# Kernel optimization log

Hardware: AMD Instinct MI355X
Metric: run time of the kernel (lower is better)

## Reference

```python
import jax, jax.numpy as jnp
import numpy as np

B, L = 4096, 64          # batch, patch_len
OUT, KS, K = 64, 8, 4    # out_planes, kernel_size, num mixtures
STRIDE = 1
TEMP = 34.0
L_OUT = (L - KS) // STRIDE + 1   # 57
C = OUT * L_OUT                  # BN feature dim = 3648
HIDDEN = int(L * 0.5) + 1        # attention hidden planes = 33
EPS = 1e-5


def _gelu(x):
    return jax.nn.gelu(x, approximate=False)  # torch nn.GELU default = exact erf


def setup_inputs() -> dict:
    key = jax.random.key(0)
    ks = jax.random.split(key, 8)
    return {
        "x": jax.random.normal(ks[0], (B, L), jnp.float32),
        "fc1_w": jax.random.normal(ks[1], (HIDDEN, L), jnp.float32) * (2.0 / HIDDEN) ** 0.5,
        "fc2_w": jax.random.normal(ks[2], (K, HIDDEN), jnp.float32) * (2.0 / K) ** 0.5,
        "fc2_b": jnp.zeros((K,), jnp.float32),
        "weight": jax.random.normal(ks[3], (K, OUT, KS), jnp.float32) * 0.1,
        "bias": jnp.zeros((K, OUT), jnp.float32),
        "bn_gamma": jnp.ones((C,), jnp.float32),
        "bn_beta": jnp.zeros((C,), jnp.float32),
    }


def reference(x, fc1_w, fc2_w, fc2_b, weight, bias, bn_gamma, bn_beta):
    # --- attention1d: 1x1 convs over the patch_len 'channel' dim == linears ---
    a = _gelu(x @ fc1_w.T)                 # [B, HIDDEN]
    logits = a @ fc2_w.T + fc2_b           # [B, K]
    attn = jax.nn.softmax(logits / TEMP, axis=1)

    # --- sliding windows (im2col), shared by both conv paths ---
    idx = jnp.arange(L_OUT)[:, None] * STRIDE + jnp.arange(KS)[None, :]
    frames = x[:, idx]                     # [B, L_OUT, KS]

    # --- kernel_wise: full conv with each of the K kernels ---
    kw = jnp.einsum('blc,koc->bolk', frames, weight) + bias.T[None, :, None, :]  # [B,OUT,L_OUT,K]
    kw = kw.reshape(B, C, K)

    # --- per-sample aggregated kernel + grouped (per-sample) conv ---
    agg_w = jnp.einsum('bk,koc->boc', attn, weight)      # [B, OUT, KS]
    agg_b = attn @ bias                                  # [B, OUT]
    out = jnp.einsum('blc,boc->bol', frames, agg_w) + agg_b[:, :, None]  # [B,OUT,L_OUT]
    out = out.reshape(B, C)

    # --- BN(GELU(.)) with batch statistics (training-mode BatchNorm1d) ---
    g = _gelu(out)
    m = g.mean(axis=0)
    v = g.var(axis=0)
    out = (g - m) * jax.lax.rsqrt(v + EPS) * bn_gamma + bn_beta

    g2 = _gelu(kw)                                        # [B, C, K]
    m2 = g2.mean(axis=(0, 2), keepdims=True)
    v2 = g2.var(axis=(0, 2), keepdims=True)
    kw = (g2 - m2) * jax.lax.rsqrt(v2 + EPS) * bn_gamma[None, :, None] + bn_beta[None, :, None]

    return out, attn, kw.transpose(0, 2, 1)              # [B,C], [B,K], [B,K,C]
```

## Files before the change

kernel.cpp:

```cpp
#include <hip/hip_runtime.h>
#include <cstddef>

#define B_     4096
#define L_     64
#define OUT_   64
#define KS_    8
#define KK_    4
#define LOUT_  57
#define C_     3648
#define HID_   33
#define TEMP_  34.0f
#define EPS_   1e-5f
#define NCH_   128
#define SROWS_ 32
#define NB2_   32

__device__ __forceinline__ float gelu_f(float x) {
    float e = exp2f(-2.3022083f * x * fmaf(0.044715f * x, x, 1.0f));
    return x * __builtin_amdgcn_rcpf(1.0f + e);
}

__global__ __launch_bounds__(128) void attn_kernel(
    const float* __restrict__ x, const float* __restrict__ fc1_w,
    const float* __restrict__ fc2_w, const float* __restrict__ fc2_b,
    float* __restrict__ attn_out)
{
    __shared__ float fc1s[HID_][L_];
    __shared__ float fc2s[KK_][HID_];
    __shared__ float fc2bs[KK_];
    int tid = threadIdx.x;
    for (int i = tid; i < HID_ * L_; i += 128) fc1s[i / L_][i % L_] = fc1_w[i];
    for (int i = tid; i < KK_ * HID_; i += 128) fc2s[i / HID_][i % HID_] = fc2_w[i];
    if (tid < KK_) fc2bs[tid] = fc2_b[tid];
    __syncthreads();

    int b = blockIdx.x * 128 + tid;
    if (b >= B_) return;

    float xr[L_];
    const float4* xp = (const float4*)(x + (size_t)b * L_);
    #pragma unroll
    for (int i = 0; i < L_ / 4; ++i) {
        float4 v = xp[i];
        xr[4*i] = v.x; xr[4*i+1] = v.y; xr[4*i+2] = v.z; xr[4*i+3] = v.w;
    }
    float logit[KK_] = {0.f, 0.f, 0.f, 0.f};
    for (int h = 0; h < HID_; ++h) {
        const float4* fr = (const float4*)&fc1s[h][0];
        float acc = 0.f;
        #pragma unroll
        for (int i = 0; i < L_ / 4; ++i) {
            float4 wv = fr[i];
            acc = fmaf(xr[4*i],   wv.x, acc);
            acc = fmaf(xr[4*i+1], wv.y, acc);
            acc = fmaf(xr[4*i+2], wv.z, acc);
            acc = fmaf(xr[4*i+3], wv.w, acc);
        }
        float a = gelu_f(acc);
        #pragma unroll
        for (int k = 0; k < KK_; ++k) logit[k] = fmaf(a, fc2s[k][h], logit[k]);
    }
    float z[KK_];
    #pragma unroll
    for (int k = 0; k < KK_; ++k) z[k] = (logit[k] + fc2bs[k]) * (1.0f / TEMP_);
    float mx = fmaxf(fmaxf(z[0], z[1]), fmaxf(z[2], z[3]));
    float e[KK_]; float s = 0.f;
    #pragma unroll
    for (int k = 0; k < KK_; ++k) { e[k] = __expf(z[k] - mx); s += e[k]; }
    float inv = __builtin_amdgcn_rcpf(s);
    #pragma unroll
    for (int k = 0; k < KK_; ++k) attn_out[(size_t)b * KK_ + k] = e[k] * inv;
}

__global__ __launch_bounds__(256) void stats_kernel(
    const float* __restrict__ x, const float* __restrict__ weight,
    const float* __restrict__ bias, const float* __restrict__ attn,
    float* __restrict__ P, int use_partial)
{
    const int RPC = B_ / NCH_;
    int cb = blockIdx.x;
    int chunk = blockIdx.y;
    int tid = threadIdx.x;
    int c = cb * 256 + tid;
    bool act = c < C_;
    int o = act ? (c / LOUT_) : 0;
    int l = act ? (c - o * LOUT_) : 0;

    float w[KK_][KS_];
    float bk[KK_];
    #pragma unroll
    for (int k = 0; k < KK_; ++k) {
        bk[k] = bias[k * OUT_ + o];
        #pragma unroll
        for (int cq = 0; cq < KS_; ++cq) w[k][cq] = weight[(k * OUT_ + o) * KS_ + cq];
    }

    __shared__ float xs[SROWS_][L_];
    __shared__ float at[SROWS_][KK_];

    float s1 = 0.f, s2 = 0.f, t1 = 0.f, t2 = 0.f;

    for (int round = 0; round < RPC / SROWS_; ++round) {
        int b0 = chunk * RPC + round * SROWS_;
        __syncthreads();
        {
            const float4* xp4 = (const float4*)(x + (size_t)b0 * L_);
            float4* xd = (float4*)&xs[0][0];
            xd[tid] = xp4[tid];
            xd[tid + 256] = xp4[tid + 256];
            if (tid < SROWS_ * KK_) ((float*)at)[tid] = attn[(size_t)b0 * KK_ + tid];
        }
        __syncthreads();
        if (act) {
            #pragma unroll 4
            for (int r = 0; r < SROWS_; ++r) {
                float kv0 = bk[0], kv1 = bk[1], kv2 = bk[2], kv3 = bk[3];
                #pragma unroll
                for (int cq = 0; cq < KS_; ++cq) {
                    float xv = xs[r][l + cq];
                    kv0 = fmaf(xv, w[0][cq], kv0);
                    kv1 = fmaf(xv, w[1][cq], kv1);
                    kv2 = fmaf(xv, w[2][cq], kv2);
                    kv3 = fmaf(xv, w[3][cq], kv3);
                }
                float ov = at[r][0] * kv0;
                ov = fmaf(at[r][1], kv1, ov);
                ov = fmaf(at[r][2], kv2, ov);
                ov = fmaf(at[r][3], kv3, ov);
                float g = gelu_f(ov);
                s1 += g; s2 = fmaf(g, g, s2);
                float g0 = gelu_f(kv0), g1 = gelu_f(kv1), g2 = gelu_f(kv2), g3 = gelu_f(kv3);
                t1 += g0 + g1 + g2 + g3;
                t2 = fmaf(g0, g0, t2); t2 = fmaf(g1, g1, t2);
                t2 = fmaf(g2, g2, t2); t2 = fmaf(g3, g3, t2);
            }
        }
    }
    if (!act) return;
    if (use_partial) {
        size_t base = (size_t)chunk * 4 * C_ + c;
        P[base]          = s1;
        P[base + C_]     = s2;
        P[base + 2 * C_] = t1;
        P[base + 3 * C_] = t2;
    } else {
        atomicAdd(&P[c], s1);
        atomicAdd(&P[C_ + c], s2);
        atomicAdd(&P[2 * C_ + c], t1);
        atomicAdd(&P[3 * C_ + c], t2);
    }
}

__global__ __launch_bounds__(256) void finalize_kernel(
    const float* __restrict__ P, const float* __restrict__ gamma,
    const float* __restrict__ beta, float* __restrict__ F, int use_partial)
{
    __shared__ float red[4][64];
    int t = threadIdx.x;
    int cl = t & 63;
    int s = t >> 6;
    int c = blockIdx.x * 64 + cl;
    float a = 0.f;
    if (use_partial) {
        for (int ch = 0; ch < NCH_; ++ch)
            a += P[((size_t)ch * 4 + s) * C_ + c];
    } else {
        a = P[(size_t)s * C_ + c];
    }
    red[s][cl] = a;
    __syncthreads();
    if (t < 64) {
        float a0 = red[0][cl], a1 = red[1][cl], a2 = red[2][cl], a3 = red[3][cl];
        float m  = a0 * (1.0f / B_);
        float v  = a1 * (1.0f / B_) - m * m;
        float rs = rsqrtf(v + EPS_);
        float m2 = a2 * (1.0f / (B_ * KK_));
        float v2 = a3 * (1.0f / (B_ * KK_)) - m2 * m2;
        float rs2 = rsqrtf(v2 + EPS_);
        float ga = gamma[c], be = beta[c];
        F[c]          = rs * ga;
        F[C_ + c]     = be - m * rs * ga;
        F[2 * C_ + c] = rs2 * ga;
        F[3 * C_ + c] = be - m2 * rs2 * ga;
    }
}

__global__ __launch_bounds__(256) void write_kernel(
    const float* __restrict__ x, const float* __restrict__ weight,
    const float* __restrict__ bias, const float* __restrict__ attn,
    const float* __restrict__ F,
    float* __restrict__ out0, float* __restrict__ kwout)
{
    int cc = blockIdx.x;
    int bg = blockIdx.y;
    int tid = threadIdx.x;
    int c = cc * 256 + tid;
    bool act = c < C_;
    int o = act ? (c / LOUT_) : 0;
    int l = act ? (c - o * LOUT_) : 0;

    float w[KK_][KS_];
    float bk[KK_];
    #pragma unroll
    for (int k = 0; k < KK_; ++k) {
        bk[k] = bias[k * OUT_ + o];
        #pragma unroll
        for (int cq = 0; cq < KS_; ++cq) w[k][cq] = weight[(k * OUT_ + o) * KS_ + cq];
    }
    float sA = 0.f, hA = 0.f, sK = 0.f, hK = 0.f;
    if (act) {
        sA = F[c]; hA = F[C_ + c]; sK = F[2 * C_ + c]; hK = F[3 * C_ + c];
    }

    __shared__ float xs[NB2_][L_];
    __shared__ float at[NB2_][KK_];
    int b0 = bg * NB2_;
    {
        const float4* xp4 = (const float4*)(x + (size_t)b0 * L_);
        float4* xd = (float4*)&xs[0][0];
        xd[tid] = xp4[tid];
        xd[tid + 256] = xp4[tid + 256];
        if (tid < NB2_ * KK_) ((float*)at)[tid] = attn[(size_t)b0 * KK_ + tid];
    }
    __syncthreads();

    if (!act) return;

    #pragma unroll 4
    for (int r = 0; r < NB2_; ++r) {
        float kv0 = bk[0], kv1 = bk[1], kv2 = bk[2], kv3 = bk[3];
        #pragma unroll
        for (int cq = 0; cq < KS_; ++cq) {
            float xv = xs[r][l + cq];
            kv0 = fmaf(xv, w[0][cq], kv0);
            kv1 = fmaf(xv, w[1][cq], kv1);
            kv2 = fmaf(xv, w[2][cq], kv2);
            kv3 = fmaf(xv, w[3][cq], kv3);
        }
        float ov = at[r][0] * kv0;
        ov = fmaf(at[r][1], kv1, ov);
        ov = fmaf(at[r][2], kv2, ov);
        ov = fmaf(at[r][3], kv3, ov);
        int b = b0 + r;
        float g = gelu_f(ov);
        out0[(size_t)b * C_ + c] = fmaf(g, sA, hA);
        float g0 = gelu_f(kv0), g1 = gelu_f(kv1), g2v = gelu_f(kv2), g3 = gelu_f(kv3);
        float* base = kwout + (size_t)b * KK_ * C_ + c;
        base[0]      = fmaf(g0,  sK, hK);
        base[C_]     = fmaf(g1,  sK, hK);
        base[2 * C_] = fmaf(g2v, sK, hK);
        base[3 * C_] = fmaf(g3,  sK, hK);
    }
}

extern "C" void kernel_launch(void* const* d_in, const int* in_sizes, int n_in,
                              void* d_out, int out_size, void* d_ws, size_t ws_size,
                              hipStream_t stream) {
    const float* x      = (const float*)d_in[0];
    const float* fc1_w  = (const float*)d_in[1];
    const float* fc2_w  = (const float*)d_in[2];
    const float* fc2_b  = (const float*)d_in[3];
    const float* weight = (const float*)d_in[4];
    const float* bias   = (const float*)d_in[5];
    const float* gamma  = (const float*)d_in[6];
    const float* beta   = (const float*)d_in[7];

    float* out  = (float*)d_out;
    float* out0 = out;
    float* attn = out + (size_t)B_ * C_;
    float* kwout = attn + (size_t)B_ * KK_;

    size_t need = (size_t)(NCH_ * 4 + 4) * C_ * sizeof(float);
    int use_partial = ws_size >= need;
    float* P = (float*)d_ws;
    float* F = P + (use_partial ? (size_t)NCH_ * 4 * C_ : (size_t)4 * C_);
    if (!use_partial)
        hipMemsetAsync(P, 0, 4 * C_ * sizeof(float), stream);

    attn_kernel<<<B_ / 128, 128, 0, stream>>>(x, fc1_w, fc2_w, fc2_b, attn);
    stats_kernel<<<dim3((C_ + 255) / 256, NCH_), 256, 0, stream>>>(
        x, weight, bias, attn, P, use_partial);
    finalize_kernel<<<C_ / 64, 256, 0, stream>>>(P, gamma, beta, F, use_partial);
    write_kernel<<<dim3((C_ + 255) / 256, B_ / NB2_), 256, 0, stream>>>(
        x, weight, bias, attn, F, out0, kwout);
}
```

Before: 147.2 us.

## Compute four adjacent output positions per thread with vectorized loads and stores

Each thread in the stats and write kernels now handles a tile of four consecutive output positions (15 tiles per output channel, the last holding a single position). It reads three float4 window segments from shared memory and reuses them across the four positions, then writes 16-byte vector stores through an unaligned packed type. The stats kernel drops its inner round loop, so each block covers only 16 rows and there are 256 chunks. The write kernel now uses 16-row groups. The trade-off is higher register pressure and partially idle last tiles, in exchange for fewer shared-memory loads and wider global stores.

```diff
diff --git a/kernel.cpp b/kernel.cpp
--- a/kernel.cpp
+++ b/kernel.cpp
@@ -11,13 +11,35 @@
 #define HID_   33
 #define TEMP_  34.0f
 #define EPS_   1e-5f
-#define NCH_   128
-#define SROWS_ 32
-#define NB2_   32
+#define NCH_   256
+#define SROWS_ 16
+#define NBW_   16
+#define NTILE_ 960
+
+typedef float f32x4 __attribute__((ext_vector_type(4)));
+
+struct __attribute__((packed, aligned(4))) f4u { f32x4 v; };
+__device__ __forceinline__ void store4(float* p, f32x4 v) {
+    reinterpret_cast<f4u*>(p)->v = v;
+}
+__device__ __forceinline__ f32x4 load4(const float* p) {
+    return reinterpret_cast<const f4u*>(p)->v;
+}
 
 __device__ __forceinline__ float gelu_f(float x) {
     float e = exp2f(-2.3022083f * x * fmaf(0.044715f * x, x, 1.0f));
     return x * __builtin_amdgcn_rcpf(1.0f + e);
+}
+
+template<int ROWS>
+__device__ __forceinline__ void stage_rows(
+    const float* __restrict__ x, int b0, int tid, float4 (*xs)[17])
+{
+    for (int idx = tid; idx < ROWS * 17; idx += 256) {
+        int r = idx / 17, t = idx - r * 17;
+        const float4* xrow = (const float4*)(x + (size_t)(b0 + r) * L_);
+        xs[r][t] = xrow[t < 16 ? t : 15];
+    }
 }
 
 __global__ __launch_bounds__(128) void attn_kernel(
@@ -35,7 +57,6 @@
     __syncthreads();
 
     int b = blockIdx.x * 128 + tid;
-    if (b >= B_) return;
 
     float xr[L_];
     const float4* xp = (const float4*)(x + (size_t)b * L_);
@@ -77,14 +98,15 @@
     const float* __restrict__ bias, const float* __restrict__ attn,
     float* __restrict__ P, int use_partial)
 {
-    const int RPC = B_ / NCH_;
-    int cb = blockIdx.x;
+    int tid = threadIdx.x;
+    int tile = blockIdx.x * 256 + tid;
     int chunk = blockIdx.y;
-    int tid = threadIdx.x;
-    int c = cb * 256 + tid;
-    bool act = c < C_;
-    int o = act ? (c / LOUT_) : 0;
-    int l = act ? (c - o * LOUT_) : 0;
+    bool act = tile < NTILE_;
+    int o  = act ? tile / 15 : 0;
+    int lt = act ? tile - o * 15 : 0;
+    int l0 = lt * 4;
+    int c0 = o * LOUT_ + l0;
+    bool full = (lt != 14);
 
     float w[KK_][KS_];
     float bk[KK_];
@@ -92,62 +114,75 @@
     for (int k = 0; k < KK_; ++k) {
         bk[k] = bias[k * OUT_ + o];
         #pragma unroll
-        for (int cq = 0; cq < KS_; ++cq) w[k][cq] = weight[(k * OUT_ + o) * KS_ + cq];
-    }
-
-    __shared__ float xs[SROWS_][L_];
-    __shared__ float at[SROWS_][KK_];
-
-    float s1 = 0.f, s2 = 0.f, t1 = 0.f, t2 = 0.f;
-
-    for (int round = 0; round < RPC / SROWS_; ++round) {
-        int b0 = chunk * RPC + round * SROWS_;
-        __syncthreads();
-        {
-            const float4* xp4 = (const float4*)(x + (size_t)b0 * L_);
-            float4* xd = (float4*)&xs[0][0];
-            xd[tid] = xp4[tid];
-            xd[tid + 256] = xp4[tid + 256];
-            if (tid < SROWS_ * KK_) ((float*)at)[tid] = attn[(size_t)b0 * KK_ + tid];
-        }
-        __syncthreads();
-        if (act) {
-            #pragma unroll 4
-            for (int r = 0; r < SROWS_; ++r) {
-                float kv0 = bk[0], kv1 = bk[1], kv2 = bk[2], kv3 = bk[3];
+        for (int t = 0; t < KS_; ++t) w[k][t] = weight[(k * OUT_ + o) * KS_ + t];
+    }
+
+    __shared__ float4 xs[SROWS_][17];
+    __shared__ float4 at4[SROWS_];
+    int b0 = chunk * SROWS_;
+    stage_rows<SROWS_>(x, b0, tid, xs);
+    if (tid < SROWS_) at4[tid] = *(const float4*)(attn + (size_t)(b0 + tid) * KK_);
+    __syncthreads();
+
+    f32x4 s1 = {0,0,0,0}, s2 = {0,0,0,0}, t1 = {0,0,0,0}, t2 = {0,0,0,0};
+    if (act) {
+        #pragma unroll 2
+        for (int r = 0; r < SROWS_; ++r) {
+            float4 X0 = xs[r][lt], X1 = xs[r][lt+1], X2 = xs[r][lt+2];
+            float xw[12] = {X0.x,X0.y,X0.z,X0.w, X1.x,X1.y,X1.z,X1.w,
+                            X2.x,X2.y,X2.z,X2.w};
+            float4 atv = at4[r];
+            float kv[4][KK_];
+            #pragma unroll
+            for (int e = 0; e < 4; ++e)
                 #pragma unroll
-                for (int cq = 0; cq < KS_; ++cq) {
-                    float xv = xs[r][l + cq];
-                    kv0 = fmaf(xv, w[0][cq], kv0);
-                    kv1 = fmaf(xv, w[1][cq], kv1);
-                    kv2 = fmaf(xv, w[2][cq], kv2);
-                    kv3 = fmaf(xv, w[3][cq], kv3);
+                for (int k = 0; k < KK_; ++k) {
+                    float a = bk[k];
+                    #pragma unroll
+                    for (int t = 0; t < KS_; ++t) a = fmaf(xw[e + t], w[k][t], a);
+                    kv[e][k] = a;
                 }
-                float ov = at[r][0] * kv0;
-                ov = fmaf(at[r][1], kv1, ov);
-                ov = fmaf(at[r][2], kv2, ov);
-                ov = fmaf(at[r][3], kv3, ov);
-                float g = gelu_f(ov);
-                s1 += g; s2 = fmaf(g, g, s2);
-                float g0 = gelu_f(kv0), g1 = gelu_f(kv1), g2 = gelu_f(kv2), g3 = gelu_f(kv3);
-                t1 += g0 + g1 + g2 + g3;
-                t2 = fmaf(g0, g0, t2); t2 = fmaf(g1, g1, t2);
-                t2 = fmaf(g2, g2, t2); t2 = fmaf(g3, g3, t2);
+            f32x4 g4;
+            #pragma unroll
+            for (int e = 0; e < 4; ++e) {
+                float ov = atv.x * kv[e][0];
+                ov = fmaf(atv.y, kv[e][1], ov);
+                ov = fmaf(atv.z, kv[e][2], ov);
+                ov = fmaf(atv.w, kv[e][3], ov);
+                g4[e] = gelu_f(ov);
+            }
+            s1 = s1 + g4;
+            s2 = __builtin_elementwise_fma(g4, g4, s2);
+            #pragma unroll
+            for (int k = 0; k < KK_; ++k) {
+                f32x4 gk;
+                #pragma unroll
+                for (int e = 0; e < 4; ++e) gk[e] = gelu_f(kv[e][k]);
+                t1 = t1 + gk;
+                t2 = __builtin_elementwise_fma(gk, gk, t2);
             }
         }
     }
     if (!act) return;
     if (use_partial) {
-        size_t base = (size_t)chunk * 4 * C_ + c;
-        P[base]          = s1;
-        P[base + C_]     = s2;
-        P[base + 2 * C_] = t1;
-        P[base + 3 * C_] = t2;
+        size_t base = (size_t)chunk * 4 * C_ + c0;
+        if (full) {
+            store4(&P[base], s1);
+            store4(&P[base + C_], s2);
+            store4(&P[base + 2 * C_], t1);
+            store4(&P[base + 3 * C_], t2);
+        } else {
+            P[base] = s1.x; P[base + C_] = s2.x;
+            P[base + 2 * C_] = t1.x; P[base + 3 * C_] = t2.x;
+        }
     } else {
-        atomicAdd(&P[c], s1);
-        atomicAdd(&P[C_ + c], s2);
-        atomicAdd(&P[2 * C_ + c], t1);
-        atomicAdd(&P[3 * C_ + c], t2);
+        int ne = full ? 4 : 1;
+        for (int e = 0; e < ne; ++e) {
+            atomicAdd(&P[c0 + e], s1[e]);
+            atomicAdd(&P[C_ + c0 + e], s2[e]);
+            atomicAdd(&P[2 * C_ + c0 + e], t1[e]);
+            atomicAdd(&P[3 * C_ + c0 + e], t2[e]);
+        }
     }
 }
 
@@ -191,13 +226,14 @@
     const float* __restrict__ F,
     float* __restrict__ out0, float* __restrict__ kwout)
 {
-    int cc = blockIdx.x;
-    int bg = blockIdx.y;
     int tid = threadIdx.x;
-    int c = cc * 256 + tid;
-    bool act = c < C_;
-    int o = act ? (c / LOUT_) : 0;
-    int l = act ? (c - o * LOUT_) : 0;
+    int tile = blockIdx.x * 256 + tid;
+    bool act = tile < NTILE_;
+    int o  = act ? tile / 15 : 0;
+    int lt = act ? tile - o * 15 : 0;
+    int l0 = lt * 4;
+    int c0 = o * LOUT_ + l0;
+    bool full = (lt != 14);
 
     float w[KK_][KS_];
     float bk[KK_];
@@ -205,51 +241,73 @@
     for (int k = 0; k < KK_; ++k) {
         bk[k] = bias[k * OUT_ + o];
         #pragma unroll
-        for (int cq = 0; cq < KS_; ++cq) w[k][cq] = weight[(k * OUT_ + o) * KS_ + cq];
-    }
-    float sA = 0.f, hA = 0.f, sK = 0.f, hK = 0.f;
+        for (int t = 0; t < KS_; ++t) w[k][t] = weight[(k * OUT_ + o) * KS_ + t];
+    }
+    f32x4 sA = {0,0,0,0}, hA = {0,0,0,0}, sK = {0,0,0,0}, hK = {0,0,0,0};
     if (act) {
-        sA = F[c]; hA = F[C_ + c]; sK = F[2 * C_ + c]; hK = F[3 * C_ + c];
-    }
-
-    __shared__ float xs[NB2_][L_];
-    __shared__ float at[NB2_][KK_];
-    int b0 = bg * NB2_;
-    {
-        const float4* xp4 = (const float4*)(x + (size_t)b0 * L_);
-        float4* xd = (float4*)&xs[0][0];
-        xd[tid] = xp4[tid];
-        xd[tid + 256] = xp4[tid + 256];
-        if (tid < NB2_ * KK_) ((float*)at)[tid] = attn[(size_t)b0 * KK_ + tid];
-    }
+        sA = load4(F + c0); hA = load4(F + C_ + c0);
+        sK = load4(F + 2 * C_ + c0); hK = load4(F + 3 * C_ + c0);
+    }
+
+    __shared__ float4 xs[NBW_][17];
+    __shared__ float4 at4[NBW_];
+    int b0 = blockIdx.y * NBW_;
+    stage_rows<NBW_>(x, b0, tid, xs);
+    if (tid < NBW_) at4[tid] = *(const float4*)(attn + (size_t)(b0 + tid) * KK_);
     __syncthreads();
 
     if (!act) return;
 
-    #pragma unroll 4
-    for (int r = 0; r < NB2_; ++r) {
-        float kv0 = bk[0], kv1 = bk[1], kv2 = bk[2], kv3 = bk[3];
-        #pragma unroll
-        for (int cq = 0; cq < KS_; ++cq) {
-            float xv = xs[r][l + cq];
-            kv0 = fmaf(xv, w[0][cq], kv0);
-            kv1 = fmaf(xv, w[1][cq], kv1);
-            kv2 = fmaf(xv, w[2][cq], kv2);
-            kv3 = fmaf(xv, w[3][cq], kv3);
-        }
-        float ov = at[r][0] * kv0;
-        ov = fmaf(at[r][1], kv1, ov);
-        ov = fmaf(at[r][2], kv2, ov);
-        ov = fmaf(at[r][3], kv3, ov);
+    #pragma unroll 2
+    for (int r = 0; r < NBW_; ++r) {
+        float4 X0 = xs[r][lt], X1 = xs[r][lt+1], X2 = xs[r][lt+2];
+        float xw[12] = {X0.x,X0.y,X0.z,X0.w, X1.x,X1.y,X1.z,X1.w,
+                        X2.x,X2.y,X2.z,X2.w};
+        float4 atv = at4[r];
+        float kv[4][KK_];
+        #pragma unroll
+        for (int e = 0; e < 4; ++e)
+            #pragma unroll
+            for (int k = 0; k < KK_; ++k) {
+                float a = bk[k];
+                #pragma unroll
+                for (int t = 0; t < KS_; ++t) a = fmaf(xw[e + t], w[k][t], a);
+                kv[e][k] = a;
+            }
+        f32x4 oo;
+        #pragma unroll
+        for (int e = 0; e < 4; ++e) {
+            float ov = atv.x * kv[e][0];
+            ov = fmaf(atv.y, kv[e][1], ov);
+            ov = fmaf(atv.z, kv[e][2], ov);
+            ov = fmaf(atv.w, kv[e][3], ov);
+            float g = gelu_f(ov);
+            oo[e] = fmaf(g, sA[e], hA[e]);
+        }
+        f32x4 kwv[KK_];
+        #pragma unroll
+        for (int k = 0; k < KK_; ++k) {
+            f32x4 gk;
+            #pragma unroll
+            for (int e = 0; e < 4; ++e) gk[e] = gelu_f(kv[e][k]);
+            kwv[k] = __builtin_elementwise_fma(gk, sK, hK);
+        }
         int b = b0 + r;
-        float g = gelu_f(ov);
-        out0[(size_t)b * C_ + c] = fmaf(g, sA, hA);
-        float g0 = gelu_f(kv0), g1 = gelu_f(kv1), g2v = gelu_f(kv2), g3 = gelu_f(kv3);
-        float* base = kwout + (size_t)b * KK_ * C_ + c;
-        base[0]      = fmaf(g0,  sK, hK);
-        base[C_]     = fmaf(g1,  sK, hK);
-        base[2 * C_] = fmaf(g2v, sK, hK);
-        base[3 * C_] = fmaf(g3,  sK, hK);
+        float* po = out0 + (size_t)b * C_ + c0;
+        float* pb = kwout + (size_t)b * KK_ * C_ + c0;
+        if (full) {
+            store4(po, oo);
+            store4(pb, kwv[0]);
+            store4(pb + C_, kwv[1]);
+            store4(pb + 2 * C_, kwv[2]);
+            store4(pb + 3 * C_, kwv[3]);
+        } else {
+            po[0] = oo.x;
+            pb[0] = kwv[0].x;
+            pb[C_] = kwv[1].x;
+            pb[2 * C_] = kwv[2].x;
+            pb[3 * C_] = kwv[3].x;
+        }
     }
 }
 
@@ -278,9 +336,9 @@
         hipMemsetAsync(P, 0, 4 * C_ * sizeof(float), stream);
 
     attn_kernel<<<B_ / 128, 128, 0, stream>>>(x, fc1_w, fc2_w, fc2_b, attn);
-    stats_kernel<<<dim3((C_ + 255) / 256, NCH_), 256, 0, stream>>>(
+    stats_kernel<<<dim3(4, NCH_), 256, 0, stream>>>(
         x, weight, bias, attn, P, use_partial);
     finalize_kernel<<<C_ / 64, 256, 0, stream>>>(P, gamma, beta, F, use_partial);
-    write_kernel<<<dim3((C_ + 255) / 256, B_ / NB2_), 256, 0, stream>>>(
+    write_kernel<<<dim3(4, B_ / NBW_), 256, 0, stream>>>(
         x, weight, bias, attn, F, out0, kwout);
 }
```

Result: slower. 152.4 us (+3.5%).
